# Performance work log

Measured on AMD Instinct MI355X. Metric: run time of the kernel, lower is better.

## Reference

```python
import jax, jax.numpy as jnp
import numpy as np

THRESHOLD = 0.5


def setup_inputs() -> dict:
    key = jax.random.key(0)
    T, B = 2048, 4096
    x = jax.random.uniform(key, (T, B, 2), dtype=jnp.float32)  # push/pop signals in [0,1]
    state0 = jnp.zeros((B, 2), dtype=jnp.float32)  # [count, tanh(count)]
    return {"x": x, "state0": state0}


def _step(state, xt):
    # state: [B, 2] = [count, tanh(count)]; xt: [B, 2] = [push, pop]
    push_sig = xt[..., 0]
    pop_sig = xt[..., 1]
    is_push = (push_sig >= THRESHOLD) & (push_sig >= pop_sig)
    is_pop = (pop_sig >= THRESHOLD) & (pop_sig > push_sig)
    delta = jnp.where(is_push, 1.0, jnp.where(is_pop, -1.0, 0.0))
    count = state[..., 0] + delta
    new_state = jnp.stack([count, jnp.tanh(count)], axis=-1)
    return new_state, new_state


def reference(x, state0):
    # x: [T, B, 2], state0: [B, 2] -> all per-step states [T, B, 2]
    _, states = jax.lax.scan(_step, state0, x)
    return states
```

## Files before the change

### kernel.cpp

```cpp
#include <hip/hip_runtime.h>
#include <math.h>

#define T_TOTAL 2048
#define B_TOTAL 4096
#define B2      (B_TOTAL / 2)
#define NCHUNK  64
#define TCHUNK  (T_TOTAL / NCHUNK)

typedef float fvec4 __attribute__((ext_vector_type(4)));

__device__ __forceinline__ int delta_of(float p, float q) {
    return (p >= 0.5f && p >= q) ? 1 : ((q >= 0.5f && q > p) ? -1 : 0);
}

__device__ __forceinline__ float fast_tanh(float x) {
    float e = __builtin_amdgcn_exp2f(x * 2.885390081777927f);
    return 1.0f - 2.0f / (e + 1.0f);
}

__device__ __forceinline__ int sext2(unsigned int bits2) {
    return ((int)(bits2 << 30)) >> 30;
}

__global__ void __launch_bounds__(256)
scan_pass1(const fvec4* __restrict__ x4,
           int2* __restrict__ partial,
           ulonglong2* __restrict__ packed) {
    const int p = blockIdx.x * blockDim.x + threadIdx.x;
    const int c = blockIdx.y;
    const int t0 = c * TCHUNK;

    int s0 = 0, s1 = 0;
    unsigned long long w0 = 0ull, w1 = 0ull;

#pragma unroll
    for (int t = 0; t < 16; ++t) {
        fvec4 v = x4[(size_t)(t0 + t) * B2 + p];
        int d0 = delta_of(v.x, v.y);
        int d1 = delta_of(v.z, v.w);
        s0 += d0; s1 += d1;
        unsigned int nib = (unsigned int)(d0 & 3) | ((unsigned int)(d1 & 3) << 2);
        w0 |= (unsigned long long)nib << (4 * t);
    }
#pragma unroll
    for (int t = 16; t < 32; ++t) {
        fvec4 v = x4[(size_t)(t0 + t) * B2 + p];
        int d0 = delta_of(v.x, v.y);
        int d1 = delta_of(v.z, v.w);
        s0 += d0; s1 += d1;
        unsigned int nib = (unsigned int)(d0 & 3) | ((unsigned int)(d1 & 3) << 2);
        w1 |= (unsigned long long)nib << (4 * (t - 16));
    }

    ulonglong2 w; w.x = w0; w.y = w1;
    packed[(size_t)c * B2 + p] = w;
    int2 s; s.x = s0; s.y = s1;
    partial[(size_t)c * B2 + p] = s;
}

__global__ void __launch_bounds__(256)
scan_emit(const int2* __restrict__ partial,
          const ulonglong2* __restrict__ packed,
          fvec4* __restrict__ o4) {
    const int p = blockIdx.x * blockDim.x + threadIdx.x;
    const int c = blockIdx.y;
    const int t0 = c * TCHUNK;

    int c0 = 0, c1 = 0;
    for (int cc = 0; cc < c; ++cc) {
        int2 v = partial[(size_t)cc * B2 + p];
        c0 += v.x; c1 += v.y;
    }

    ulonglong2 w = packed[(size_t)c * B2 + p];

#pragma unroll
    for (int t = 0; t < 16; ++t) {
        unsigned int nib = (unsigned int)(w.x >> (4 * t)) & 0xFu;
        c0 += sext2(nib & 3u);
        c1 += sext2(nib >> 2);
        float f0 = (float)c0, f1 = (float)c1;
        fvec4 o; o.x = f0; o.y = fast_tanh(f0); o.z = f1; o.w = fast_tanh(f1);
        o4[(size_t)(t0 + t) * B2 + p] = o;
    }
#pragma unroll
    for (int t = 16; t < 32; ++t) {
        unsigned int nib = (unsigned int)(w.y >> (4 * (t - 16))) & 0xFu;
        c0 += sext2(nib & 3u);
        c1 += sext2(nib >> 2);
        float f0 = (float)c0, f1 = (float)c1;
        fvec4 o; o.x = f0; o.y = fast_tanh(f0); o.z = f1; o.w = fast_tanh(f1);
        o4[(size_t)(t0 + t) * B2 + p] = o;
    }
}

__global__ void naive_scan(const float* __restrict__ x, float* __restrict__ out) {
    const int b = blockIdx.x * blockDim.x + threadIdx.x;
    if (b >= B_TOTAL) return;
    const float2* __restrict__ x2 = (const float2*)x;
    float2* __restrict__ o2 = (float2*)out;
    int count = 0;
    for (int t = 0; t < T_TOTAL; ++t) {
        float2 v = x2[(size_t)t * B_TOTAL + b];
        count += delta_of(v.x, v.y);
        float fc = (float)count;
        float2 w; w.x = fc; w.y = tanhf(fc);
        o2[(size_t)t * B_TOTAL + b] = w;
    }
}

extern "C" void kernel_launch(void* const* d_in, const int* in_sizes, int n_in,
                              void* d_out, int out_size, void* d_ws, size_t ws_size,
                              hipStream_t stream) {
    const float* x = (const float*)d_in[0];
    float* out = (float*)d_out;

    const size_t partial_bytes = (size_t)NCHUNK * B2 * sizeof(int2);
    const size_t packed_bytes  = (size_t)NCHUNK * B2 * sizeof(ulonglong2);
    if (ws_size < partial_bytes + packed_bytes) {
        naive_scan<<<dim3((B_TOTAL + 255) / 256), dim3(256), 0, stream>>>(x, out);
        return;
    }
    int2* partial = (int2*)d_ws;
    ulonglong2* packed = (ulonglong2*)((char*)d_ws + partial_bytes);

    dim3 block(256);
    dim3 grid(B2 / 256, NCHUNK);
    scan_pass1<<<grid, block, 0, stream>>>((const fvec4*)x, partial, packed);
    scan_emit<<<grid, block, 0, stream>>>(partial, packed, (fvec4*)out);
}
```

Baseline: 116.4 us.

## Fuse chunked scan passes into one kernel with shared-memory chunk sums

Replaces the two-kernel chunked scan with a single kernel. Each block owns 4 column-pairs across all 64 time chunks and exchanges chunk partial sums through shared memory. This removes the second launch, the global workspace writes and reads of partials and packed deltas, and the O(chunks) global prefix loop. In exchange, global accesses shrink to 64-byte contiguous segments per timestep, and the grid drops to 512 blocks, which may hurt coalescing and latency hiding. The naive workspace-free fallback path is also removed.

```diff
diff --git a/kernel.cpp b/kernel.cpp
--- a/kernel.cpp
+++ b/kernel.cpp
@@ -4,6 +4,7 @@
 #define T_TOTAL 2048
 #define B_TOTAL 4096
 #define B2      (B_TOTAL / 2)
+#define PPB     4
 #define NCHUNK  64
 #define TCHUNK  (T_TOTAL / NCHUNK)
 
@@ -23,12 +24,14 @@
 }
 
 __global__ void __launch_bounds__(256)
-scan_pass1(const fvec4* __restrict__ x4,
-           int2* __restrict__ partial,
-           ulonglong2* __restrict__ packed) {
-    const int p = blockIdx.x * blockDim.x + threadIdx.x;
-    const int c = blockIdx.y;
-    const int t0 = c * TCHUNK;
+scan_fused(const fvec4* __restrict__ x4, fvec4* __restrict__ o4) {
+    const int tid = threadIdx.x;
+    const int pl  = tid & (PPB - 1);
+    const int ch  = tid >> 2;
+    const int p   = blockIdx.x * PPB + pl;
+    const int t0  = ch * TCHUNK;
+
+    __shared__ int2 sums[NCHUNK * PPB];
 
     int s0 = 0, s1 = 0;
     unsigned long long w0 = 0ull, w1 = 0ull;
@@ -52,31 +55,19 @@
         w1 |= (unsigned long long)nib << (4 * (t - 16));
     }
 
-    ulonglong2 w; w.x = w0; w.y = w1;
-    packed[(size_t)c * B2 + p] = w;
     int2 s; s.x = s0; s.y = s1;
-    partial[(size_t)c * B2 + p] = s;
-}
-
-__global__ void __launch_bounds__(256)
-scan_emit(const int2* __restrict__ partial,
-          const ulonglong2* __restrict__ packed,
-          fvec4* __restrict__ o4) {
-    const int p = blockIdx.x * blockDim.x + threadIdx.x;
-    const int c = blockIdx.y;
-    const int t0 = c * TCHUNK;
+    sums[tid] = s;
+    __syncthreads();
 
     int c0 = 0, c1 = 0;
-    for (int cc = 0; cc < c; ++cc) {
-        int2 v = partial[(size_t)cc * B2 + p];
+    for (int cc = 0; cc < ch; ++cc) {
+        int2 v = sums[cc * PPB + pl];
         c0 += v.x; c1 += v.y;
     }
 
-    ulonglong2 w = packed[(size_t)c * B2 + p];
-
 #pragma unroll
     for (int t = 0; t < 16; ++t) {
-        unsigned int nib = (unsigned int)(w.x >> (4 * t)) & 0xFu;
+        unsigned int nib = (unsigned int)(w0 >> (4 * t)) & 0xFu;
         c0 += sext2(nib & 3u);
         c1 += sext2(nib >> 2);
         float f0 = (float)c0, f1 = (float)c1;
@@ -85,7 +76,7 @@
     }
 #pragma unroll
     for (int t = 16; t < 32; ++t) {
-        unsigned int nib = (unsigned int)(w.y >> (4 * (t - 16))) & 0xFu;
+        unsigned int nib = (unsigned int)(w1 >> (4 * (t - 16))) & 0xFu;
         c0 += sext2(nib & 3u);
         c1 += sext2(nib >> 2);
         float f0 = (float)c0, f1 = (float)c1;
@@ -94,38 +85,10 @@
     }
 }
 
-__global__ void naive_scan(const float* __restrict__ x, float* __restrict__ out) {
-    const int b = blockIdx.x * blockDim.x + threadIdx.x;
-    if (b >= B_TOTAL) return;
-    const float2* __restrict__ x2 = (const float2*)x;
-    float2* __restrict__ o2 = (float2*)out;
-    int count = 0;
-    for (int t = 0; t < T_TOTAL; ++t) {
-        float2 v = x2[(size_t)t * B_TOTAL + b];
-        count += delta_of(v.x, v.y);
-        float fc = (float)count;
-        float2 w; w.x = fc; w.y = tanhf(fc);
-        o2[(size_t)t * B_TOTAL + b] = w;
-    }
-}
-
 extern "C" void kernel_launch(void* const* d_in, const int* in_sizes, int n_in,
                               void* d_out, int out_size, void* d_ws, size_t ws_size,
                               hipStream_t stream) {
-    const float* x = (const float*)d_in[0];
-    float* out = (float*)d_out;
-
-    const size_t partial_bytes = (size_t)NCHUNK * B2 * sizeof(int2);
-    const size_t packed_bytes  = (size_t)NCHUNK * B2 * sizeof(ulonglong2);
-    if (ws_size < partial_bytes + packed_bytes) {
-        naive_scan<<<dim3((B_TOTAL + 255) / 256), dim3(256), 0, stream>>>(x, out);
-        return;
-    }
-    int2* partial = (int2*)d_ws;
-    ulonglong2* packed = (ulonglong2*)((char*)d_ws + partial_bytes);
-
-    dim3 block(256);
-    dim3 grid(B2 / 256, NCHUNK);
-    scan_pass1<<<grid, block, 0, stream>>>((const fvec4*)x, partial, packed);
-    scan_emit<<<grid, block, 0, stream>>>(partial, packed, (fvec4*)out);
+    const fvec4* x4 = (const fvec4*)d_in[0];
+    fvec4* o4 = (fvec4*)d_out;
+    scan_fused<<<dim3(B2 / PPB), dim3(256), 0, stream>>>(x4, o4);
 }
```

Measured after the change: 135.3 us. 1.16x slower.
